# Kernel tuning notes

Measured on AMD Instinct MI355X. Metric: run time of the kernel, lower is better.

The kernel has to match this reference:

```python
import jax, jax.numpy as jnp
import numpy as np

DIM = 1024
NUM_EXPERTS = 8
TOP_K = 2
HIDDEN = int(DIM * 1.5)  # 1536, matches expert_dim = int(dim * 1.5)


def setup_inputs() -> dict:
    key = jax.random.key(0)
    k_x, k_r, k_w1, k_w2, k_w3 = jax.random.split(key, 5)
    B, T = 2, 4096
    s_in = 1.0 / np.sqrt(DIM)
    s_h = 1.0 / np.sqrt(HIDDEN)
    return {
        "x": jax.random.normal(k_x, (B, T, DIM), dtype=jnp.float32),
        # router: Linear(dim, num_experts, bias=False) -> stored as [C, E]
        "Wr": jax.random.uniform(k_r, (DIM, NUM_EXPERTS), minval=-s_in, maxval=s_in, dtype=jnp.float32),
        # stacked expert weights: w1/w3 [E, C, H], w2 [E, H, C]
        "W1": jax.random.uniform(k_w1, (NUM_EXPERTS, DIM, HIDDEN), minval=-s_in, maxval=s_in, dtype=jnp.float32),
        "W2": jax.random.uniform(k_w2, (NUM_EXPERTS, HIDDEN, DIM), minval=-s_h, maxval=s_h, dtype=jnp.float32),
        "W3": jax.random.uniform(k_w3, (NUM_EXPERTS, DIM, HIDDEN), minval=-s_in, maxval=s_in, dtype=jnp.float32),
    }


def reference(x, Wr, W1, W2, W3):
    B, T, C = x.shape
    xf = x.reshape(-1, C)  # [N, C]
    gate_logits = xf @ Wr  # [N, E]
    w, idx = jax.lax.top_k(gate_logits, TOP_K)  # [N, K]
    w = jax.nn.softmax(w, axis=-1)
    # dense combine weights: zero for non-selected experts -> [N, E]
    comb = jnp.sum(w[:, :, None] * jax.nn.one_hot(idx, NUM_EXPERTS, dtype=w.dtype), axis=1)
    # SwiGLU for all experts (masked-out experts contribute with weight 0)
    h = jnp.einsum('nc,ech->neh', xf, W1)  # [N, E, H]
    g = jnp.einsum('nc,ech->neh', xf, W3)  # [N, E, H]
    y = jnp.einsum('neh,ehc->nec', jax.nn.silu(h) * g, W2)  # [N, E, C]
    out = jnp.einsum('nec,ne->nc', y, comb)
    return out.reshape(B, T, C)
```

## Files before the change

### kernel.cpp

```cpp
#include <hip/hip_runtime.h>
#include <hip/hip_bf16.h>
#include <math.h>

#define DIM   1024
#define NEXP  8
#define HID   1536
#define NTOK  8192
#define NPOS  16384
#define PADR  128

typedef __attribute__((ext_vector_type(8))) short bf16x8;
typedef __attribute__((ext_vector_type(4))) float floatx4;

__device__ __forceinline__ unsigned short f2bf(float f) {
  unsigned int u = __float_as_uint(f);
  u += 0x7FFFu + ((u >> 16) & 1u);
  return (unsigned short)(u >> 16);
}

__device__ __forceinline__ float bf2f(unsigned short h) {
  return __uint_as_float((unsigned int)h << 16);
}

__device__ __forceinline__ void async_cp16(void* lds, const void* g) {
  __builtin_amdgcn_global_load_lds(
      (const __attribute__((address_space(1))) unsigned int*)g,
      (__attribute__((address_space(3))) unsigned int*)lds, 16, 0, 0);
}

__device__ __forceinline__ int2 cnt_off(const int* __restrict__ hdr, int e) {
  int s = 0, c = 0;
#pragma unroll
  for (int i = 0; i < NEXP; ++i) {
    const int v = hdr[i];
    if (i < e) s += v;
    if (i == e) c = v;
  }
  return make_int2(c, s);
}

__global__ __launch_bounds__(256) void moe_router(
    const float* __restrict__ x, const float* __restrict__ Wr,
    int* __restrict__ meta_e, float* __restrict__ meta_w) {
  const int wave = threadIdx.x >> 6, lane = threadIdx.x & 63;
  const int token = blockIdx.x * 4 + wave;
  const float* xr = x + (size_t)token * DIM;
  float acc[NEXP];
#pragma unroll
  for (int e = 0; e < NEXP; ++e) acc[e] = 0.f;
  for (int i = lane; i < DIM; i += 64) {
    const float xv = xr[i];
    const float* wr = Wr + (size_t)i * NEXP;
#pragma unroll
    for (int e = 0; e < NEXP; ++e) acc[e] += xv * wr[e];
  }
#pragma unroll
  for (int off = 32; off > 0; off >>= 1) {
#pragma unroll
    for (int e = 0; e < NEXP; ++e) acc[e] += __shfl_down(acc[e], off);
  }
  if (lane == 0) {
    int i0 = 0; float v0 = acc[0];
#pragma unroll
    for (int e = 1; e < NEXP; ++e) if (acc[e] > v0) { v0 = acc[e]; i0 = e; }
    int i1 = -1; float v1 = -3.4e38f;
#pragma unroll
    for (int e = 0; e < NEXP; ++e) if (e != i0 && acc[e] > v1) { v1 = acc[e]; i1 = e; }
    const float w0 = 1.f / (1.f + expf(v1 - v0));
    meta_e[token * 2 + 0] = i0;
    meta_e[token * 2 + 1] = i1;
    meta_w[token * 2 + 0] = w0;
    meta_w[token * 2 + 1] = 1.f - w0;
  }
}

__global__ __launch_bounds__(256) void moe_hist(
    const int* __restrict__ meta_e, int* __restrict__ hdr) {
  const int idx = blockIdx.x * 256 + threadIdx.x;
  const int lane = threadIdx.x & 63;
  const int e = meta_e[idx];
#pragma unroll
  for (int ex = 0; ex < NEXP; ++ex) {
    const unsigned long long m = __ballot(e == ex);
    if (m && lane == 0) atomicAdd(&hdr[ex], __popcll(m));
  }
}

__global__ __launch_bounds__(256) void moe_build(
    const int* __restrict__ meta_e, int* __restrict__ hdr,
    int* __restrict__ tok, int* __restrict__ inv) {
  const int idx = blockIdx.x * 256 + threadIdx.x;
  const int lane = threadIdx.x & 63;
  const int token = idx >> 1;
  const int e = meta_e[idx];
  int pos = 0;
#pragma unroll
  for (int ex = 0; ex < NEXP; ++ex) {
    const unsigned long long m = __ballot(e == ex);
    if (m) {
      const int leader = (int)__ffsll((long long)m) - 1;
      int base = 0;
      if (lane == leader) base = atomicAdd(&hdr[16 + ex], __popcll(m));
      base = __shfl(base, leader);
      if (e == ex) {
        const int2 co = cnt_off(hdr, ex);
        pos = co.y + base + (int)__popcll(m & ((1ull << lane) - 1ull));
      }
    }
  }
  tok[pos] = token;
  inv[idx] = pos;
}

__global__ __launch_bounds__(256) void moe_gather(
    const float* __restrict__ x, const int* __restrict__ tok,
    unsigned short* __restrict__ Xg) {
  const int pos = blockIdx.x;
  const int t = tok[pos];
  const float4 v = ((const float4*)(x + (size_t)t * DIM))[threadIdx.x];
  ushort4 o = make_ushort4(f2bf(v.x), f2bf(v.y), f2bf(v.z), f2bf(v.w));
  ((ushort4*)(Xg + (size_t)pos * DIM))[threadIdx.x] = o;
}

__global__ __launch_bounds__(256) void moe_transpose_all(
    const float* __restrict__ W1, const float* __restrict__ W3,
    const float* __restrict__ W2,
    unsigned short* __restrict__ W1t, unsigned short* __restrict__ W3t,
    unsigned short* __restrict__ W2t) {
  __shared__ float tile[32][33];
  const int z = blockIdx.z;
  const int which = z >> 3, e = z & 7;
  const float* src; unsigned short* dst; int R, C;
  if (which == 0)      { src = W1; dst = W1t; R = DIM; C = HID; }
  else if (which == 1) { src = W3; dst = W3t; R = DIM; C = HID; }
  else                 { src = W2; dst = W2t; R = HID; C = DIM; }
  const int nbx = C / 32;
  const int bx = blockIdx.x % nbx, by = blockIdx.x / nbx;
  const float* ein = src + (size_t)e * R * C;
  unsigned short* eout = dst + (size_t)e * R * C;
  const int c0 = bx * 32, r0 = by * 32;
  const int tx = threadIdx.x, ty = threadIdx.y;
#pragma unroll
  for (int rr = ty; rr < 32; rr += 8)
    tile[rr][tx] = ein[(size_t)(r0 + rr) * C + c0 + tx];
  __syncthreads();
#pragma unroll
  for (int cc = ty; cc < 32; cc += 8)
    eout[(size_t)(c0 + cc) * R + r0 + tx] = f2bf(tile[tx][cc]);
}

__global__ __launch_bounds__(256) void moe_gemm1(
    const unsigned short* __restrict__ Xg,
    const unsigned short* __restrict__ W1t,
    const unsigned short* __restrict__ W3t,
    unsigned short* __restrict__ Hbuf,
    const int* __restrict__ hdr) {
  const int e = blockIdx.y;
  const int NT = HID / 64;
  const int tileRow = blockIdx.x / NT;
  const int tileN = blockIdx.x % NT;
  const int2 co = cnt_off(hdr, e);
  const int cnt = co.x;
  if (tileRow * 128 >= cnt) return;
  const int off = co.y;
  const size_t tileM = (size_t)off + (size_t)tileRow * 128;
  const int n0 = tileN * 64;

  __shared__ unsigned short As[128 * 32];
  __shared__ unsigned short B1s[64 * 32];
  __shared__ unsigned short B3s[64 * 32];

  const int lane = threadIdx.x & 63;
  const int wave = threadIdx.x >> 6;
  const int wm = wave >> 1, wn = wave & 1;
  const int rsub = lane >> 2;
  const int ksub = (lane & 3) * 8;

  const unsigned short* Abase = Xg + tileM * DIM;
  const unsigned short* B1base = W1t + ((size_t)e * HID + n0) * DIM;
  const unsigned short* B3base = W3t + ((size_t)e * HID + n0) * DIM;

  floatx4 zero = {0.f, 0.f, 0.f, 0.f};
  floatx4 acc_h[4][2], acc_g[4][2];
#pragma unroll
  for (int i = 0; i < 4; ++i)
#pragma unroll
    for (int j = 0; j < 2; ++j) { acc_h[i][j] = zero; acc_g[i][j] = zero; }

  for (int k0 = 0; k0 < DIM; k0 += 32) {
    {
#pragma unroll
      for (int t = 0; t < 2; ++t) {
        const int c = wave * 2 + t;
        const int row = c * 16 + rsub;
        async_cp16(&As[c * 512], Abase + (size_t)row * DIM + k0 + ksub);
      }
      const int row = wave * 16 + rsub;
      async_cp16(&B1s[wave * 512], B1base + (size_t)row * DIM + k0 + ksub);
      async_cp16(&B3s[wave * 512], B3base + (size_t)row * DIM + k0 + ksub);
    }
    __syncthreads();
    bf16x8 a[4], b1[2], b3[2];
#pragma unroll
    for (int i = 0; i < 4; ++i)
      a[i] = *(const bf16x8*)&As[(wm * 64 + i * 16 + (lane & 15)) * 32 + (lane >> 4) * 8];
#pragma unroll
    for (int j = 0; j < 2; ++j) {
      b1[j] = *(const bf16x8*)&B1s[(wn * 32 + j * 16 + (lane & 15)) * 32 + (lane >> 4) * 8];
      b3[j] = *(const bf16x8*)&B3s[(wn * 32 + j * 16 + (lane & 15)) * 32 + (lane >> 4) * 8];
    }
#pragma unroll
    for (int i = 0; i < 4; ++i)
#pragma unroll
      for (int j = 0; j < 2; ++j) {
        acc_h[i][j] = __builtin_amdgcn_mfma_f32_16x16x32_bf16(a[i], b1[j], acc_h[i][j], 0, 0, 0);
        acc_g[i][j] = __builtin_amdgcn_mfma_f32_16x16x32_bf16(a[i], b3[j], acc_g[i][j], 0, 0, 0);
      }
    __syncthreads();
  }

  const int r0 = (lane >> 4) * 4;
  const int cc = lane & 15;
#pragma unroll
  for (int i = 0; i < 4; ++i)
#pragma unroll
    for (int r = 0; r < 4; ++r) {
      const int lrow = tileRow * 128 + wm * 64 + i * 16 + r0 + r;
      if (lrow < cnt) {
        unsigned short* hrow = Hbuf + (size_t)(off + lrow) * HID + n0 + wn * 32 + cc;
#pragma unroll
        for (int j = 0; j < 2; ++j) {
          const float h = acc_h[i][j][r];
          const float g = acc_g[i][j][r];
          const float s = h / (1.f + expf(-h));
          hrow[j * 16] = f2bf(s * g);
        }
      }
    }
}

__global__ __launch_bounds__(256) void moe_gemm2(
    const unsigned short* __restrict__ Hbuf,
    const unsigned short* __restrict__ W2t,
    const int* __restrict__ hdr,
    unsigned short* __restrict__ Y) {
  const int e = blockIdx.y;
  const int NT = DIM / 128;
  const int tileRow = blockIdx.x / NT;
  const int tileN = blockIdx.x % NT;
  const int2 co = cnt_off(hdr, e);
  const int cnt = co.x;
  if (tileRow * 128 >= cnt) return;
  const int off = co.y;
  const size_t tileM = (size_t)off + (size_t)tileRow * 128;
  const int n0 = tileN * 128;

  __shared__ unsigned short As[128 * 32];
  __shared__ unsigned short Bs[128 * 32];

  const int lane = threadIdx.x & 63;
  const int wave = threadIdx.x >> 6;
  const int wm = wave >> 1, wn = wave & 1;
  const int rsub = lane >> 2;
  const int ksub = (lane & 3) * 8;

  const unsigned short* Abase = Hbuf + tileM * HID;
  const unsigned short* Bbase = W2t + ((size_t)e * DIM + n0) * HID;

  floatx4 zero = {0.f, 0.f, 0.f, 0.f};
  floatx4 acc[4][4];
#pragma unroll
  for (int i = 0; i < 4; ++i)
#pragma unroll
    for (int j = 0; j < 4; ++j) acc[i][j] = zero;

  for (int k0 = 0; k0 < HID; k0 += 32) {
#pragma unroll
    for (int t = 0; t < 2; ++t) {
      const int c = wave * 2 + t;
      const int row = c * 16 + rsub;
      const size_t goff = (size_t)row * HID + k0 + ksub;
      async_cp16(&As[c * 512], Abase + goff);
      async_cp16(&Bs[c * 512], Bbase + goff);
    }
    __syncthreads();
    bf16x8 a[4], b[4];
#pragma unroll
    for (int i = 0; i < 4; ++i)
      a[i] = *(const bf16x8*)&As[(wm * 64 + i * 16 + (lane & 15)) * 32 + (lane >> 4) * 8];
#pragma unroll
    for (int j = 0; j < 4; ++j)
      b[j] = *(const bf16x8*)&Bs[(wn * 64 + j * 16 + (lane & 15)) * 32 + (lane >> 4) * 8];
#pragma unroll
    for (int i = 0; i < 4; ++i)
#pragma unroll
      for (int j = 0; j < 4; ++j)
        acc[i][j] = __builtin_amdgcn_mfma_f32_16x16x32_bf16(a[i], b[j], acc[i][j], 0, 0, 0);
    __syncthreads();
  }

  const int r0 = (lane >> 4) * 4;
  const int cc = lane & 15;
#pragma unroll
  for (int i = 0; i < 4; ++i)
#pragma unroll
    for (int r = 0; r < 4; ++r) {
      const int lrow = tileRow * 128 + wm * 64 + i * 16 + r0 + r;
      if (lrow < cnt) {
        unsigned short* yrow = Y + (size_t)(off + lrow) * DIM + n0 + wn * 64 + cc;
#pragma unroll
        for (int j = 0; j < 4; ++j)
          yrow[j * 16] = f2bf(acc[i][j][r]);
      }
    }
}

__global__ __launch_bounds__(256) void moe_combine(
    const unsigned short* __restrict__ Y, const int* __restrict__ inv,
    const float* __restrict__ meta_w, float* __restrict__ out) {
  const int t = blockIdx.x;
  const int p0 = inv[t * 2 + 0], p1 = inv[t * 2 + 1];
  const float w0 = meta_w[t * 2 + 0], w1 = meta_w[t * 2 + 1];
  const ushort4 a = ((const ushort4*)(Y + (size_t)p0 * DIM))[threadIdx.x];
  const ushort4 b = ((const ushort4*)(Y + (size_t)p1 * DIM))[threadIdx.x];
  float4 o;
  o.x = w0 * bf2f(a.x) + w1 * bf2f(b.x);
  o.y = w0 * bf2f(a.y) + w1 * bf2f(b.y);
  o.z = w0 * bf2f(a.z) + w1 * bf2f(b.z);
  o.w = w0 * bf2f(a.w) + w1 * bf2f(b.w);
  ((float4*)(out + (size_t)t * DIM))[threadIdx.x] = o;
}

extern "C" void kernel_launch(void* const* d_in, const int* in_sizes, int n_in,
                              void* d_out, int out_size, void* d_ws, size_t ws_size,
                              hipStream_t stream) {
  const float* x  = (const float*)d_in[0];
  const float* Wr = (const float*)d_in[1];
  const float* W1 = (const float*)d_in[2];
  const float* W2 = (const float*)d_in[3];
  const float* W3 = (const float*)d_in[4];
  float* out = (float*)d_out;

  char* p = (char*)d_ws;
  auto carve = [&](size_t bytes) { char* r = p; p += (bytes + 255) & ~(size_t)255; return r; };

  int*            hdr    = (int*)carve(256);
  int*            meta_e = (int*)carve((size_t)NTOK * 2 * sizeof(int));
  float*          meta_w = (float*)carve((size_t)NTOK * 2 * sizeof(float));
  int*            tok    = (int*)carve((size_t)NPOS * sizeof(int));
  int*            inv    = (int*)carve((size_t)NTOK * 2 * sizeof(int));
  unsigned short* Xg     = (unsigned short*)carve((size_t)(NPOS + PADR) * DIM * 2);
  unsigned short* Hbuf   = (unsigned short*)carve((size_t)(NPOS + PADR) * HID * 2);
  unsigned short* W1t    = (unsigned short*)carve((size_t)NEXP * HID * DIM * 2);
  unsigned short* W3t    = (unsigned short*)carve((size_t)NEXP * HID * DIM * 2);
  unsigned short* W2t    = (unsigned short*)carve((size_t)NEXP * DIM * HID * 2);
  unsigned short* Y      = Xg;

  hipMemsetAsync(hdr, 0, 256, stream);

  moe_router<<<NTOK / 4, 256, 0, stream>>>(x, Wr, meta_e, meta_w);
  moe_hist<<<NPOS / 256, 256, 0, stream>>>(meta_e, hdr);
  moe_build<<<NPOS / 256, 256, 0, stream>>>(meta_e, hdr, tok, inv);
  moe_gather<<<NPOS, 256, 0, stream>>>(x, tok, Xg);

  moe_transpose_all<<<dim3(1536, 1, 24), dim3(32, 8), 0, stream>>>(W1, W3, W2, W1t, W3t, W2t);

  moe_gemm1<<<dim3(64 * (HID / 64), NEXP), 256, 0, stream>>>(Xg, W1t, W3t, Hbuf, hdr);
  moe_gemm2<<<dim3(64 * (DIM / 128), NEXP), 256, 0, stream>>>(Hbuf, W2t, hdr, Y);
  moe_combine<<<NTOK, 256, 0, stream>>>(Y, inv, meta_w, out);
}
```

Measured before the change: 552.2 us.

## Widen GEMM K-tiles to 64, shrink gemm2 N-tile, vectorize weight transpose

Both expert GEMMs now stage 64-wide K slices in LDS and run two MFMA sub-steps per barrier pair, halving the number of sync/load rounds. gemm2's output tile narrows from 128 to 64 columns, doubling its block count and halving accumulators per thread. The weight transpose uses 64x64 tiles with float4 loads and ushort4 stores instead of scalar accesses. The trade-off is more LDS per block, possible LDS bank conflicts from the row stride of 64 bf16 elements, and gemm2 re-reading the A tile for twice as many N tiles.

```diff
diff --git a/kernel.cpp b/kernel.cpp
--- a/kernel.cpp
+++ b/kernel.cpp
@@ -127,26 +127,36 @@
     const float* __restrict__ W2,
     unsigned short* __restrict__ W1t, unsigned short* __restrict__ W3t,
     unsigned short* __restrict__ W2t) {
-  __shared__ float tile[32][33];
+  __shared__ float tile[64][65];
   const int z = blockIdx.z;
   const int which = z >> 3, e = z & 7;
   const float* src; unsigned short* dst; int R, C;
   if (which == 0)      { src = W1; dst = W1t; R = DIM; C = HID; }
   else if (which == 1) { src = W3; dst = W3t; R = DIM; C = HID; }
   else                 { src = W2; dst = W2t; R = HID; C = DIM; }
-  const int nbx = C / 32;
+  const int nbx = C / 64;
   const int bx = blockIdx.x % nbx, by = blockIdx.x / nbx;
   const float* ein = src + (size_t)e * R * C;
   unsigned short* eout = dst + (size_t)e * R * C;
-  const int c0 = bx * 32, r0 = by * 32;
-  const int tx = threadIdx.x, ty = threadIdx.y;
-#pragma unroll
-  for (int rr = ty; rr < 32; rr += 8)
-    tile[rr][tx] = ein[(size_t)(r0 + rr) * C + c0 + tx];
+  const int c0 = bx * 64, r0 = by * 64;
+  const int lx = threadIdx.x & 15, ly = threadIdx.x >> 4;
+#pragma unroll
+  for (int it = 0; it < 4; ++it) {
+    const int r = ly + it * 16;
+    const float4 v = *(const float4*)&ein[(size_t)(r0 + r) * C + c0 + lx * 4];
+    tile[r][lx * 4 + 0] = v.x;
+    tile[r][lx * 4 + 1] = v.y;
+    tile[r][lx * 4 + 2] = v.z;
+    tile[r][lx * 4 + 3] = v.w;
+  }
   __syncthreads();
 #pragma unroll
-  for (int cc = ty; cc < 32; cc += 8)
-    eout[(size_t)(c0 + cc) * R + r0 + tx] = f2bf(tile[tx][cc]);
+  for (int it = 0; it < 4; ++it) {
+    const int cc = ly + it * 16;
+    ushort4 o = make_ushort4(f2bf(tile[lx * 4 + 0][cc]), f2bf(tile[lx * 4 + 1][cc]),
+                             f2bf(tile[lx * 4 + 2][cc]), f2bf(tile[lx * 4 + 3][cc]));
+    *(ushort4*)&eout[(size_t)(c0 + cc) * R + r0 + lx * 4] = o;
+  }
 }
 
 __global__ __launch_bounds__(256) void moe_gemm1(
@@ -166,15 +176,15 @@
   const size_t tileM = (size_t)off + (size_t)tileRow * 128;
   const int n0 = tileN * 64;
 
-  __shared__ unsigned short As[128 * 32];
-  __shared__ unsigned short B1s[64 * 32];
-  __shared__ unsigned short B3s[64 * 32];
+  __shared__ unsigned short As[128 * 64];
+  __shared__ unsigned short B1s[64 * 64];
+  __shared__ unsigned short B3s[64 * 64];
 
   const int lane = threadIdx.x & 63;
   const int wave = threadIdx.x >> 6;
   const int wm = wave >> 1, wn = wave & 1;
-  const int rsub = lane >> 2;
-  const int ksub = (lane & 3) * 8;
+  const int rsub8 = lane >> 3;
+  const int ksub8 = (lane & 7) * 8;
 
   const unsigned short* Abase = Xg + tileM * DIM;
   const unsigned short* B1base = W1t + ((size_t)e * HID + n0) * DIM;
@@ -187,35 +197,41 @@
 #pragma unroll
     for (int j = 0; j < 2; ++j) { acc_h[i][j] = zero; acc_g[i][j] = zero; }
 
-  for (int k0 = 0; k0 < DIM; k0 += 32) {
-    {
-#pragma unroll
-      for (int t = 0; t < 2; ++t) {
-        const int c = wave * 2 + t;
-        const int row = c * 16 + rsub;
-        async_cp16(&As[c * 512], Abase + (size_t)row * DIM + k0 + ksub);
+  for (int k0 = 0; k0 < DIM; k0 += 64) {
+#pragma unroll
+    for (int t = 0; t < 4; ++t) {
+      const int c = wave * 4 + t;
+      const int row = c * 8 + rsub8;
+      async_cp16(&As[c * 512], Abase + (size_t)row * DIM + k0 + ksub8);
+    }
+#pragma unroll
+    for (int t = 0; t < 2; ++t) {
+      const int c = wave * 2 + t;
+      const int row = c * 8 + rsub8;
+      async_cp16(&B1s[c * 512], B1base + (size_t)row * DIM + k0 + ksub8);
+      async_cp16(&B3s[c * 512], B3base + (size_t)row * DIM + k0 + ksub8);
+    }
+    __syncthreads();
+#pragma unroll
+    for (int s = 0; s < 2; ++s) {
+      bf16x8 a[4], b1[2], b3[2];
+      const int ko = s * 32 + (lane >> 4) * 8;
+#pragma unroll
+      for (int i = 0; i < 4; ++i)
+        a[i] = *(const bf16x8*)&As[(wm * 64 + i * 16 + (lane & 15)) * 64 + ko];
+#pragma unroll
+      for (int j = 0; j < 2; ++j) {
+        b1[j] = *(const bf16x8*)&B1s[(wn * 32 + j * 16 + (lane & 15)) * 64 + ko];
+        b3[j] = *(const bf16x8*)&B3s[(wn * 32 + j * 16 + (lane & 15)) * 64 + ko];
       }
-      const int row = wave * 16 + rsub;
-      async_cp16(&B1s[wave * 512], B1base + (size_t)row * DIM + k0 + ksub);
-      async_cp16(&B3s[wave * 512], B3base + (size_t)row * DIM + k0 + ksub);
-    }
-    __syncthreads();
-    bf16x8 a[4], b1[2], b3[2];
-#pragma unroll
-    for (int i = 0; i < 4; ++i)
-      a[i] = *(const bf16x8*)&As[(wm * 64 + i * 16 + (lane & 15)) * 32 + (lane >> 4) * 8];
-#pragma unroll
-    for (int j = 0; j < 2; ++j) {
-      b1[j] = *(const bf16x8*)&B1s[(wn * 32 + j * 16 + (lane & 15)) * 32 + (lane >> 4) * 8];
-      b3[j] = *(const bf16x8*)&B3s[(wn * 32 + j * 16 + (lane & 15)) * 32 + (lane >> 4) * 8];
-    }
-#pragma unroll
-    for (int i = 0; i < 4; ++i)
-#pragma unroll
-      for (int j = 0; j < 2; ++j) {
-        acc_h[i][j] = __builtin_amdgcn_mfma_f32_16x16x32_bf16(a[i], b1[j], acc_h[i][j], 0, 0, 0);
-        acc_g[i][j] = __builtin_amdgcn_mfma_f32_16x16x32_bf16(a[i], b3[j], acc_g[i][j], 0, 0, 0);
-      }
+#pragma unroll
+      for (int i = 0; i < 4; ++i)
+#pragma unroll
+        for (int j = 0; j < 2; ++j) {
+          acc_h[i][j] = __builtin_amdgcn_mfma_f32_16x16x32_bf16(a[i], b1[j], acc_h[i][j], 0, 0, 0);
+          acc_g[i][j] = __builtin_amdgcn_mfma_f32_16x16x32_bf16(a[i], b3[j], acc_g[i][j], 0, 0, 0);
+        }
+    }
     __syncthreads();
   }
 
@@ -245,7 +261,7 @@
     const int* __restrict__ hdr,
     unsigned short* __restrict__ Y) {
   const int e = blockIdx.y;
-  const int NT = DIM / 128;
+  const int NT = DIM / 64;
   const int tileRow = blockIdx.x / NT;
   const int tileN = blockIdx.x % NT;
   const int2 co = cnt_off(hdr, e);
@@ -253,49 +269,57 @@
   if (tileRow * 128 >= cnt) return;
   const int off = co.y;
   const size_t tileM = (size_t)off + (size_t)tileRow * 128;
-  const int n0 = tileN * 128;
-
-  __shared__ unsigned short As[128 * 32];
-  __shared__ unsigned short Bs[128 * 32];
+  const int n0 = tileN * 64;
+
+  __shared__ unsigned short As[128 * 64];
+  __shared__ unsigned short Bs[64 * 64];
 
   const int lane = threadIdx.x & 63;
   const int wave = threadIdx.x >> 6;
   const int wm = wave >> 1, wn = wave & 1;
-  const int rsub = lane >> 2;
-  const int ksub = (lane & 3) * 8;
+  const int rsub8 = lane >> 3;
+  const int ksub8 = (lane & 7) * 8;
 
   const unsigned short* Abase = Hbuf + tileM * HID;
   const unsigned short* Bbase = W2t + ((size_t)e * DIM + n0) * HID;
 
   floatx4 zero = {0.f, 0.f, 0.f, 0.f};
-  floatx4 acc[4][4];
+  floatx4 acc[4][2];
 #pragma unroll
   for (int i = 0; i < 4; ++i)
 #pragma unroll
-    for (int j = 0; j < 4; ++j) acc[i][j] = zero;
-
-  for (int k0 = 0; k0 < HID; k0 += 32) {
+    for (int j = 0; j < 2; ++j) acc[i][j] = zero;
+
+  for (int k0 = 0; k0 < HID; k0 += 64) {
+#pragma unroll
+    for (int t = 0; t < 4; ++t) {
+      const int c = wave * 4 + t;
+      const int row = c * 8 + rsub8;
+      async_cp16(&As[c * 512], Abase + (size_t)row * HID + k0 + ksub8);
+    }
 #pragma unroll
     for (int t = 0; t < 2; ++t) {
       const int c = wave * 2 + t;
-      const int row = c * 16 + rsub;
-      const size_t goff = (size_t)row * HID + k0 + ksub;
-      async_cp16(&As[c * 512], Abase + goff);
-      async_cp16(&Bs[c * 512], Bbase + goff);
+      const int row = c * 8 + rsub8;
+      async_cp16(&Bs[c * 512], Bbase + (size_t)row * HID + k0 + ksub8);
     }
     __syncthreads();
-    bf16x8 a[4], b[4];
-#pragma unroll
-    for (int i = 0; i < 4; ++i)
-      a[i] = *(const bf16x8*)&As[(wm * 64 + i * 16 + (lane & 15)) * 32 + (lane >> 4) * 8];
-#pragma unroll
-    for (int j = 0; j < 4; ++j)
-      b[j] = *(const bf16x8*)&Bs[(wn * 64 + j * 16 + (lane & 15)) * 32 + (lane >> 4) * 8];
-#pragma unroll
-    for (int i = 0; i < 4; ++i)
-#pragma unroll
-      for (int j = 0; j < 4; ++j)
-        acc[i][j] = __builtin_amdgcn_mfma_f32_16x16x32_bf16(a[i], b[j], acc[i][j], 0, 0, 0);
+#pragma unroll
+    for (int s = 0; s < 2; ++s) {
+      bf16x8 a[4], b[2];
+      const int ko = s * 32 + (lane >> 4) * 8;
+#pragma unroll
+      for (int i = 0; i < 4; ++i)
+        a[i] = *(const bf16x8*)&As[(wm * 64 + i * 16 + (lane & 15)) * 64 + ko];
+#pragma unroll
+      for (int j = 0; j < 2; ++j)
+        b[j] = *(const bf16x8*)&Bs[(wn * 32 + j * 16 + (lane & 15)) * 64 + ko];
+#pragma unroll
+      for (int i = 0; i < 4; ++i)
+#pragma unroll
+        for (int j = 0; j < 2; ++j)
+          acc[i][j] = __builtin_amdgcn_mfma_f32_16x16x32_bf16(a[i], b[j], acc[i][j], 0, 0, 0);
+    }
     __syncthreads();
   }
 
@@ -307,9 +331,9 @@
     for (int r = 0; r < 4; ++r) {
       const int lrow = tileRow * 128 + wm * 64 + i * 16 + r0 + r;
       if (lrow < cnt) {
-        unsigned short* yrow = Y + (size_t)(off + lrow) * DIM + n0 + wn * 64 + cc;
-#pragma unroll
-        for (int j = 0; j < 4; ++j)
+        unsigned short* yrow = Y + (size_t)(off + lrow) * DIM + n0 + wn * 32 + cc;
+#pragma unroll
+        for (int j = 0; j < 2; ++j)
           yrow[j * 16] = f2bf(acc[i][j][r]);
       }
     }
@@ -363,9 +387,9 @@
   moe_build<<<NPOS / 256, 256, 0, stream>>>(meta_e, hdr, tok, inv);
   moe_gather<<<NPOS, 256, 0, stream>>>(x, tok, Xg);
 
-  moe_transpose_all<<<dim3(1536, 1, 24), dim3(32, 8), 0, stream>>>(W1, W3, W2, W1t, W3t, W2t);
+  moe_transpose_all<<<dim3(384, 1, 24), dim3(256), 0, stream>>>(W1, W3, W2, W1t, W3t, W2t);
 
   moe_gemm1<<<dim3(64 * (HID / 64), NEXP), 256, 0, stream>>>(Xg, W1t, W3t, Hbuf, hdr);
-  moe_gemm2<<<dim3(64 * (DIM / 128), NEXP), 256, 0, stream>>>(Hbuf, W2t, hdr, Y);
+  moe_gemm2<<<dim3(64 * (DIM / 64), NEXP), 256, 0, stream>>>(Hbuf, W2t, hdr, Y);
   moe_combine<<<NTOK, 256, 0, stream>>>(Y, inv, meta_w, out);
 }
```

New measurement: 587.2 us. 6.3% more time.
